# Kernel tuning notes

Hardware: AMD Instinct MI355X
Metric: run time of the kernel (lower is better)

Reference implementation:

```python
import jax, jax.numpy as jnp
import numpy as np

EPS = 1e-5
H = 8  # attention heads


def _bn(f, g, b):
    # MinkowskiBatchNorm: per-channel batch-norm over all N points (training stats)
    mu = f.mean(0)
    var = f.var(0)
    return g * (f - mu) * jax.lax.rsqrt(var + EPS) + b


def setup_inputs() -> dict:
    key = jax.random.key(0)
    ks = jax.random.split(key, 8)
    B, GS, ED = 8, 1024, 512
    N = B * GS
    s = 1.0 / np.sqrt(ED)
    inp = {
        "x": jax.random.normal(ks[0], (N, ED), jnp.float32),
        "mask": jnp.ones((B, GS), bool),
        "Wq": jax.random.normal(ks[1], (ED, ED), jnp.float32) * s,
        "bq": jnp.zeros((ED,), jnp.float32),
        "Wk": jax.random.normal(ks[2], (ED, ED), jnp.float32) * s,
        "bk": jnp.zeros((ED,), jnp.float32),
        "Wv": jax.random.normal(ks[3], (ED, ED), jnp.float32) * s,
        "bv": jnp.zeros((ED,), jnp.float32),
        "Wo": jax.random.normal(ks[4], (ED, ED), jnp.float32) * s,
        "bo": jnp.zeros((ED,), jnp.float32),
        "g1": jnp.ones((ED,), jnp.float32),
        "be1": jnp.zeros((ED,), jnp.float32),
        "g2": jnp.ones((ED,), jnp.float32),
        "be2": jnp.zeros((ED,), jnp.float32),
        "W1": jax.random.normal(ks[5], (ED, 4 * ED), jnp.float32) * s,
        "b1m": jnp.zeros((4 * ED,), jnp.float32),
        "W2": jax.random.normal(ks[6], (4 * ED, ED), jnp.float32) * (0.5 * s),
        "b2m": jnp.zeros((ED,), jnp.float32),
        "b": B,
        "gs": GS,
    }
    return inp


def reference(x, mask, Wq, bq, Wk, bk, Wv, bv, Wo, bo, g1, be1, g2, be2, W1, b1m, W2, b2m, b, gs):
    ed = x.shape[-1]
    dh = ed // H
    # --- pre-norm + multi-head self-attention over [b, gs] groups ---
    h1 = _bn(x, g1, be1)
    q = (h1 @ Wq + bq).reshape(b, gs, H, dh)
    k = (h1 @ Wk + bk).reshape(b, gs, H, dh)
    v = (h1 @ Wv + bv).reshape(b, gs, H, dh)
    scores = jnp.einsum('bqhd,bkhd->bhqk', q, k) / jnp.sqrt(jnp.float32(dh))
    scores = jnp.where(mask[:, None, None, :], scores, jnp.float32(-1e9))
    a = jax.nn.softmax(scores, axis=-1)
    o = jnp.einsum('bhqk,bkhd->bqhd', a, v).reshape(b * gs, ed)
    x = x + (o @ Wo + bo)  # residual (dropout identity at eval/d_rate=0)
    # --- pre-norm + MLP (GELU exact, as torch default) ---
    h2 = _bn(x, g2, be2)
    m = jax.nn.gelu(h2 @ W1 + b1m, approximate=False) @ W2 + b2m
    return x + m
```

## Files before the change

### kernel.cpp

```cpp
#include <hip/hip_runtime.h>
#include <hip/hip_bf16.h>


typedef unsigned short u16;
typedef unsigned int   u32;
typedef __attribute__((ext_vector_type(8))) short bf16x8;
typedef __attribute__((ext_vector_type(4))) float f32x4;
typedef __attribute__((ext_vector_type(4))) u16   u16x4;

#define ED   512
#define NTOK 8192
#define GSZ  1024
#define NH   8
#define DH   64

__device__ __forceinline__ u16 f2bf(float f) {
    __hip_bfloat16 h = __float2bfloat16(f);
    union { __hip_bfloat16 h; u16 u; } v; v.h = h;
    return v.u;
}

__device__ __forceinline__ void gload_lds16(const u16* g, u16* lds) {
    __builtin_amdgcn_global_load_lds(
        (const __attribute__((address_space(1))) u32*)g,
        (__attribute__((address_space(3))) u32*)lds, 16, 0, 0);
}

__device__ __forceinline__ f32x4 mfma16(bf16x8 a, bf16x8 b, f32x4 c) {
    return __builtin_amdgcn_mfma_f32_16x16x32_bf16(a, b, c, 0, 0, 0);
}

__device__ __forceinline__ float fast_gelu(float v) {
    float u = v * (0.797884560802865f + 0.0356774081f * v * v);
    float e = exp2f(u * 2.88539008177793f);
    float t = 1.f - 2.f / (1.f + e);
    return 0.5f * v * (1.f + t);
}

__device__ __forceinline__ void xcd_swizzle(int& bx, int& by) {
    int ny = gridDim.y;
    int nwg = gridDim.x * ny;
    int wg = blockIdx.y * gridDim.x + blockIdx.x;
    int per = nwg >> 3;
    int swz = (wg & 7) * per + (wg >> 3);
    by = swz % ny;
    bx = swz / ny;
}

__global__ __launch_bounds__(256) void wt_cast(const float* __restrict__ W,
                                               u16* __restrict__ Wt, int K, int N)
{
    __shared__ float t[32][33];
    int n0 = blockIdx.x * 32, k0 = blockIdx.y * 32;
    int tx = threadIdx.x & 31, ty = threadIdx.x >> 5;
#pragma unroll
    for (int r = 0; r < 4; ++r)
        t[ty * 4 + r][tx] = W[(size_t)(k0 + ty * 4 + r) * N + n0 + tx];
    __syncthreads();
#pragma unroll
    for (int r = 0; r < 4; ++r)
        Wt[(size_t)(n0 + ty * 4 + r) * K + k0 + tx] = f2bf(t[tx][ty * 4 + r]);
}

__global__ __launch_bounds__(256) void wt_cast4(
    const float* w0, const float* w1, const float* w2, const float* w3,
    u16* o0, u16* o1, u16* o2, u16* o3)
{
    const float* W = blockIdx.z == 0 ? w0 : blockIdx.z == 1 ? w1 : blockIdx.z == 2 ? w2 : w3;
    u16*        Wt = blockIdx.z == 0 ? o0 : blockIdx.z == 1 ? o1 : blockIdx.z == 2 ? o2 : o3;
    __shared__ float t[32][33];
    int n0 = blockIdx.x * 32, k0 = blockIdx.y * 32;
    int tx = threadIdx.x & 31, ty = threadIdx.x >> 5;
#pragma unroll
    for (int r = 0; r < 4; ++r)
        t[ty * 4 + r][tx] = W[(size_t)(k0 + ty * 4 + r) * ED + n0 + tx];
    __syncthreads();
#pragma unroll
    for (int r = 0; r < 4; ++r)
        Wt[(size_t)(n0 + ty * 4 + r) * ED + k0 + tx] = f2bf(t[tx][ty * 4 + r]);
}

__global__ __launch_bounds__(512) void bn_stats(const float* __restrict__ x,
                                                float* __restrict__ psum,
                                                float* __restrict__ psq)
{
    int c = threadIdx.x, blk = blockIdx.x;
    const float* p = x + (size_t)blk * 64 * ED + c;
    float s = 0.f, q = 0.f;
#pragma unroll 4
    for (int r = 0; r < 64; ++r) { float v = p[(size_t)r * ED]; s += v; q += v * v; }
    psum[blk * ED + c] = s;
    psq [blk * ED + c] = q;
}

__global__ __launch_bounds__(512) void bn_final(const float* __restrict__ psum,
                                                const float* __restrict__ psq,
                                                const float* __restrict__ g,
                                                const float* __restrict__ be,
                                                float* __restrict__ sb)
{
    int c = threadIdx.x;
    float s = 0.f, q = 0.f;
    for (int i = 0; i < 128; ++i) { s += psum[i * ED + c]; q += psq[i * ED + c]; }
    float mu  = s * (1.f / NTOK);
    float var = q * (1.f / NTOK) - mu * mu;
    float sc  = g[c] * rsqrtf(var + 1e-5f);
    sb[c]      = sc;
    sb[ED + c] = be[c] - mu * sc;
}

__global__ __launch_bounds__(256) void bn_apply(const float* __restrict__ x,
                                                const float* __restrict__ sb,
                                                u16* __restrict__ h)
{
    size_t idx = (size_t)blockIdx.x * 256 + threadIdx.x;
    const float4 v = ((const float4*)x)[idx];
    int c = (int)((idx * 4) & (ED - 1));
    u16x4 o;
    o[0] = f2bf(v.x * sb[c + 0] + sb[ED + c + 0]);
    o[1] = f2bf(v.y * sb[c + 1] + sb[ED + c + 1]);
    o[2] = f2bf(v.z * sb[c + 2] + sb[ED + c + 2]);
    o[3] = f2bf(v.w * sb[c + 3] + sb[ED + c + 3]);
    ((u16x4*)h)[idx] = o;
}

template <int BN, int BK>
__device__ __forceinline__ void gemm_core(const u16* __restrict__ A,
                                          const u16* __restrict__ Bt,
                                          int lda, int ldb, int K,
                                          size_t arow0, size_t brow0,
                                          u16 (&As)[2][128 * BK], u16 (&Bs)[2][BN * BK],
                                          f32x4 (&acc)[4][BN / 32])
{
    constexpr int NJ   = BN / 32;
    constexpr int KH   = BK / 32;
    constexpr int SEGS = BK / 8;
    constexpr int ACH  = (128 * BK) / 2048;
    constexpr int BCH  = (BN * BK) / 2048;
    const int tid  = threadIdx.x;
    const int lane = tid & 63, wid = tid >> 6;
    const int wm = wid >> 1, wn = wid & 1;
    const int frow = lane & 15, g = lane >> 4;
#pragma unroll
    for (int i = 0; i < 4; ++i)
#pragma unroll
        for (int j = 0; j < NJ; ++j) acc[i][j] = f32x4{0.f, 0.f, 0.f, 0.f};

#define SWZSEG(SG, R) ((BK == 64) ? ((SG) ^ ((R) & 7)) : ((SG) ^ (((R) >> 1) & 3)))
#define STAGE(K0, BUF) do {                                                     \
        _Pragma("unroll")                                                       \
        for (int a_ = 0; a_ < ACH; ++a_) {                                      \
            int c_ = tid + a_ * 256; int r_ = c_ / SEGS; int sg_ = c_ % SEGS;   \
            gload_lds16(A + (arow0 + r_) * lda + (K0) + SWZSEG(sg_, r_) * 8,    \
                        &As[BUF][c_ * 8]);                                      \
        }                                                                       \
        _Pragma("unroll")                                                       \
        for (int b_ = 0; b_ < BCH; ++b_) {                                      \
            int c_ = tid + b_ * 256; int r_ = c_ / SEGS; int sg_ = c_ % SEGS;   \
            gload_lds16(Bt + (brow0 + r_) * ldb + (K0) + SWZSEG(sg_, r_) * 8,   \
                        &Bs[BUF][c_ * 8]);                                      \
        }                                                                       \
    } while (0)

    STAGE(0, 0);
    __syncthreads();

    const int nt = K / BK;
    for (int t = 0; t < nt; ++t) {
        const int cur = t & 1;
        if (t + 1 < nt) STAGE((t + 1) * BK, cur ^ 1);
        const char* Ac = (const char*)&As[cur][0];
        const char* Bc = (const char*)&Bs[cur][0];
        bf16x8 af[4][KH], bfr[NJ][KH];
#pragma unroll
        for (int i = 0; i < 4; ++i) {
            int row = wm * 64 + i * 16 + frow;
#pragma unroll
            for (int kh = 0; kh < KH; ++kh) {
                int byte = row * (2 * BK) + kh * 64 + g * 16;
                byte ^= (BK == 64) ? ((row & 7) << 4) : ((row & 6) << 3);
                af[i][kh] = *(const bf16x8*)(Ac + byte);
            }
        }
#pragma unroll
        for (int j = 0; j < NJ; ++j) {
            int row = wn * (BN / 2) + j * 16 + frow;
#pragma unroll
            for (int kh = 0; kh < KH; ++kh) {
                int byte = row * (2 * BK) + kh * 64 + g * 16;
                byte ^= (BK == 64) ? ((row & 7) << 4) : ((row & 6) << 3);
                bfr[j][kh] = *(const bf16x8*)(Bc + byte);
            }
        }
#pragma unroll
        for (int kh = 0; kh < KH; ++kh)
#pragma unroll
            for (int i = 0; i < 4; ++i)
#pragma unroll
                for (int j = 0; j < NJ; ++j)
                    acc[i][j] = mfma16(af[i][kh], bfr[j][kh], acc[i][j]);
        __syncthreads();
    }
#undef STAGE
#undef SWZSEG
}

__global__ __launch_bounds__(256) void qkv_gemm(
    const u16* __restrict__ h1,
    const u16* __restrict__ wqT, const u16* __restrict__ wkT, const u16* __restrict__ wvT,
    const float* __restrict__ bq, const float* __restrict__ bk, const float* __restrict__ bv,
    u16* __restrict__ Q, u16* __restrict__ Kb, u16* __restrict__ Vt)
{
    __shared__ u16 As[2][4096];
    __shared__ u16 Bs[2][4096];
    int bx, by;
    xcd_swizzle(bx, by);
    int mb = bx;
    int which = by >> 2;
    int nloc = (by & 3) * 128;
    const u16*  Bt   = which == 0 ? wqT : (which == 1 ? wkT : wvT);
    const float* bias = which == 0 ? bq : (which == 1 ? bk : bv);
    f32x4 acc[4][4];
    gemm_core<128, 32>(h1, Bt, ED, ED, ED, (size_t)mb * 128, (size_t)nloc, As, Bs, acc);

    int lane = threadIdx.x & 63, wid = threadIdx.x >> 6;
    int wm = wid >> 1, wn = wid & 1, G = lane >> 4, r16 = lane & 15;
    int colb = nloc + wn * 64 + r16;
    float bsc[4];
#pragma unroll
    for (int j = 0; j < 4; ++j) bsc[j] = bias[colb + j * 16];

    if (which == 2) {
#pragma unroll
        for (int i = 0; i < 4; ++i) {
            int row0 = mb * 128 + wm * 64 + i * 16 + G * 4;
            int bidx = row0 >> 10, kv = row0 & (GSZ - 1);
#pragma unroll
            for (int j = 0; j < 4; ++j) {
                int col = colb + j * 16;
                int hh = col >> 6, d = col & 63;
                u16x4 pk;
#pragma unroll
                for (int r = 0; r < 4; ++r) pk[r] = f2bf(acc[i][j][r] + bsc[j]);
                *(u16x4*)(Vt + ((size_t)((bidx * NH + hh) * DH + d)) * GSZ + kv) = pk;
            }
        }
    } else {
        float scale = which == 0 ? 0.18033688011112042f : 1.0f;
        u16* Dst = which == 0 ? Q : Kb;
#pragma unroll
        for (int i = 0; i < 4; ++i) {
            int row = mb * 128 + wm * 64 + i * 16 + G * 4;
#pragma unroll
            for (int j = 0; j < 4; ++j) {
                int col = colb + j * 16;
#pragma unroll
                for (int r = 0; r < 4; ++r)
                    Dst[(size_t)(row + r) * ED + col] = f2bf((acc[i][j][r] + bsc[j]) * scale);
            }
        }
    }
}

template <int MODE, int BN, int BK>
__global__ __launch_bounds__(256) void gemm_epi(
    const u16* __restrict__ A, const u16* __restrict__ Bt, const float* __restrict__ bias,
    const float* res, float* outf, u16* outb, int K, int N)
{
    __shared__ u16 As[2][128 * BK];
    __shared__ u16 Bs[2][BN * BK];
    constexpr int NJ = BN / 32;
    int bx, by;
    xcd_swizzle(bx, by);
    f32x4 acc[4][NJ];
    gemm_core<BN, BK>(A, Bt, K, K, K, (size_t)bx * 128, (size_t)by * BN, As, Bs, acc);

    int lane = threadIdx.x & 63, wid = threadIdx.x >> 6;
    int wm = wid >> 1, wn = wid & 1, G = lane >> 4, r16 = lane & 15;
    int colb = by * BN + wn * (BN / 2) + r16;
    float bsc[NJ];
#pragma unroll
    for (int j = 0; j < NJ; ++j) bsc[j] = bias[colb + j * 16];
#pragma unroll
    for (int i = 0; i < 4; ++i) {
        int row = bx * 128 + wm * 64 + i * 16 + G * 4;
#pragma unroll
        for (int j = 0; j < NJ; ++j) {
            int col = colb + j * 16;
#pragma unroll
            for (int r = 0; r < 4; ++r) {
                float v = acc[i][j][r] + bsc[j];
                size_t o = (size_t)(row + r) * N + col;
                if (MODE == 1) {
                    outf[o] = v + res[o];
                } else {
                    outb[o] = f2bf(fast_gelu(v));
                }
            }
        }
    }
}

template <int MODE>
__global__ __launch_bounds__(512, 1) void gemm256(
    const u16* __restrict__ A, const u16* __restrict__ Bt, const float* __restrict__ bias,
    const float* res, float* outf, u16* outb, int K, int N)
{
    __shared__ u16 As[2][2][256 * 32];
    __shared__ u16 Bs[2][2][256 * 32];
    int bx, by;
    xcd_swizzle(bx, by);
    const int tid = threadIdx.x;
    const int lane = tid & 63, wid = tid >> 6;
    const int wm = wid >> 2, wn = wid & 3;
    const int frow = lane & 15, g = lane >> 4;
    const size_t arow0 = (size_t)bx * 256, brow0 = (size_t)by * 256;

    f32x4 acc[8][4];
#pragma unroll
    for (int i = 0; i < 8; ++i)
#pragma unroll
        for (int j = 0; j < 4; ++j) acc[i][j] = f32x4{0.f, 0.f, 0.f, 0.f};

#define SSLICE(KT, SL, BUF) do {                                                \
        const u16* m_ = ((SL) & 1) ? Bt : A;                                    \
        size_t rb_ = ((SL) & 1) ? brow0 : arow0;                                \
        u16* d_ = ((SL) & 1) ? &Bs[BUF][(SL) >> 1][0] : &As[BUF][(SL) >> 1][0]; \
        int kc_ = (KT) * 64 + ((SL) >> 1) * 32;                                 \
        _Pragma("unroll")                                                       \
        for (int q_ = 0; q_ < 2; ++q_) {                                        \
            int c_ = tid + q_ * 512;                                            \
            int r_ = c_ >> 2, sg_ = (c_ & 3) ^ ((r_ >> 1) & 3);                 \
            gload_lds16(m_ + (rb_ + r_) * (size_t)K + kc_ + sg_ * 8,            \
                        d_ + c_ * 8);                                           \
        }                                                                       \
    } while (0)

#define PHASE(BUF, KH, IH) do {                                                 \
        const char* Ac_ = (const char*)&As[BUF][KH][0];                         \
        const char* Bc_ = (const char*)&Bs[BUF][KH][0];                         \
        bf16x8 af_[4], bf_[4];                                                  \
        _Pragma("unroll")                                                       \
        for (int j_ = 0; j_ < 4; ++j_) {                                        \
            int row_ = wn * 64 + j_ * 16 + frow;                                \
            bf_[j_] = *(const bf16x8*)(Bc_ + row_ * 64 +                        \
                       ((g ^ ((row_ >> 1) & 3)) << 4));                         \
        }                                                                       \
        _Pragma("unroll")                                                       \
        for (int i_ = 0; i_ < 4; ++i_) {                                        \
            int row_ = wm * 128 + ((IH) * 4 + i_) * 16 + frow;                  \
            af_[i_] = *(const bf16x8*)(Ac_ + row_ * 64 +                        \
                       ((g ^ ((row_ >> 1) & 3)) << 4));                         \
        }                                                                       \
        __builtin_amdgcn_s_setprio(1);                                          \
        _Pragma("unroll")                                                       \
        for (int i_ = 0; i_ < 4; ++i_)                                          \
            _Pragma("unroll")                                                   \
            for (int j_ = 0; j_ < 4; ++j_)                                      \
                acc[(IH) * 4 + i_][j_] = mfma16(af_[i_], bf_[j_],               \
                                                acc[(IH) * 4 + i_][j_]);        \
        __builtin_amdgcn_s_setprio(0);                                          \
    } while (0)

    const int nt = K >> 6;
    SSLICE(0, 0, 0); SSLICE(0, 1, 0); SSLICE(0, 2, 0); SSLICE(0, 3, 0);
    asm volatile("s_waitcnt vmcnt(4)" ::: "memory");
    asm volatile("s_barrier" ::: "memory");

    for (int kt = 0; kt < nt; ++kt) {
        const int buf = kt & 1;
        const bool more = (kt + 1 < nt);
        if (more) SSLICE(kt + 1, 0, buf ^ 1);
        PHASE(buf, 0, 0);
        if (more) SSLICE(kt + 1, 1, buf ^ 1);
        PHASE(buf, 0, 1);
        if (more) asm volatile("s_waitcnt vmcnt(4)" ::: "memory");
        else      asm volatile("s_waitcnt vmcnt(0)" ::: "memory");
        asm volatile("s_barrier" ::: "memory");
        if (more) SSLICE(kt + 1, 2, buf ^ 1);
        PHASE(buf, 1, 0);
        if (more) SSLICE(kt + 1, 3, buf ^ 1);
        PHASE(buf, 1, 1);
        if (more) asm volatile("s_waitcnt vmcnt(4)" ::: "memory");
        else      asm volatile("s_waitcnt vmcnt(0)" ::: "memory");
        asm volatile("s_barrier" ::: "memory");
    }
#undef SSLICE
#undef PHASE

    const int G = lane >> 4, r16 = lane & 15;
    int colb = by * 256 + wn * 64 + r16;
    float bsc[4];
#pragma unroll
    for (int j = 0; j < 4; ++j) bsc[j] = bias[colb + j * 16];
#pragma unroll
    for (int i = 0; i < 8; ++i) {
        int row = bx * 256 + wm * 128 + i * 16 + G * 4;
#pragma unroll
        for (int j = 0; j < 4; ++j) {
            int col = colb + j * 16;
#pragma unroll
            for (int r = 0; r < 4; ++r) {
                float v = acc[i][j][r] + bsc[j];
                size_t o = (size_t)(row + r) * N + col;
                if (MODE == 1) {
                    outf[o] = v + res[o];
                } else {
                    outb[o] = f2bf(fast_gelu(v));
                }
            }
        }
    }
}

__global__ __launch_bounds__(512) void attn(const u16* __restrict__ Q,
                                            const u16* __restrict__ Kb,
                                            const u16* __restrict__ Vt,
                                            u16* __restrict__ O)
{
    __shared__ u16 KS[3][4096];
    __shared__ u16 VS[3][4096];
    __shared__ u16 P[8][1024];

    const int f = blockIdx.y * 8 + blockIdx.x;
    const int qt = (f >> 3) & 7;
    const int bh = ((f >> 6) << 3) + (f & 7);
    const int b = bh >> 3, h = bh & 7;
    const int tid = threadIdx.x, lane = tid & 63, w = tid >> 6;
    const int G = lane >> 4, r16 = lane & 15;
    char* Pw = (char*)&P[w][0];
    const int qbase = qt * 128 + w * 16;
    const int swz = (r16 & 7) << 4;

    const u16* kbase = Kb + ((size_t)b * GSZ) * ED + h * DH;
    const u16* vbase = Vt + ((size_t)bh * DH) * GSZ;

    const int c0 = tid;
    const int row0 = c0 >> 3, seg0 = (c0 & 7) ^ (row0 & 7);

    bf16x8 aq[2];
#pragma unroll
    for (int ks = 0; ks < 2; ++ks)
        aq[ks] = *(const bf16x8*)(Q + (size_t)(b * GSZ + qbase + r16) * ED
                                  + h * DH + ks * 32 + G * 8);

    bf16x8 ones;
#pragma unroll
    for (int i = 0; i < 8; ++i) ones[i] = (short)0x3F80;

    f32x4 o[4];
#pragma unroll
    for (int dt = 0; dt < 4; ++dt) o[dt] = f32x4{0.f, 0.f, 0.f, 0.f};
    f32x4 o_l = f32x4{0.f, 0.f, 0.f, 0.f};
    float m = -3e38f;

#define ASTAGE(C, BUF) do {                                                     \
        int kv0_ = (C) * 64;                                                    \
        gload_lds16(kbase + (size_t)(kv0_ + row0) * ED + seg0 * 8,              \
                    &KS[BUF][0] + c0 * 8);                                      \
        gload_lds16(vbase + (size_t)row0 * GSZ + kv0_ + seg0 * 8,               \
                    &VS[BUF][0] + c0 * 8);                                      \
    } while (0)

    ASTAGE(0, 0);
    ASTAGE(1, 1);
    asm volatile("s_waitcnt vmcnt(2)" ::: "memory");
    asm volatile("s_barrier" ::: "memory");

    for (int c = 0; c < 16; ++c) {
        const int cur = c % 3;
        if (c + 2 < 16) ASTAGE(c + 2, (c + 2) % 3);
        const char* Kc = (const char*)&KS[cur][0];
        const char* Vc = (const char*)&VS[cur][0];

        f32x4 s[4];
#pragma unroll
        for (int t = 0; t < 4; ++t) s[t] = f32x4{0.f, 0.f, 0.f, 0.f};
#pragma unroll
        for (int t = 0; t < 4; ++t) {
            int kvrow = (t * 16 + r16) * 128;
#pragma unroll
            for (int ks = 0; ks < 2; ++ks) {
                bf16x8 bk = *(const bf16x8*)(Kc + ((kvrow + ks * 64 + G * 16) ^ swz));
                s[t] = mfma16(bk, aq[ks], s[t]);
            }
        }

        float cm = fmaxf(fmaxf(fmaxf(s[0][0], s[0][1]), fmaxf(s[0][2], s[0][3])),
                         fmaxf(fmaxf(s[1][0], s[1][1]), fmaxf(s[1][2], s[1][3])));
        float cm2 = fmaxf(fmaxf(fmaxf(s[2][0], s[2][1]), fmaxf(s[2][2], s[2][3])),
                          fmaxf(fmaxf(s[3][0], s[3][1]), fmaxf(s[3][2], s[3][3])));
        cm = fmaxf(cm, cm2);
        if (__any(cm - m > 8.f)) {
            float mx = fmaxf(cm, __shfl_xor(cm, 16, 64));
            mx = fmaxf(mx, __shfl_xor(mx, 32, 64));
            float mn = fmaxf(m, mx);
            float r = exp2f(m - mn);
            m = mn;
            float rb[4];
#pragma unroll
            for (int j = 0; j < 4; ++j) rb[j] = __shfl(r, G * 4 + j, 64);
#pragma unroll
            for (int dt = 0; dt < 4; ++dt) {
                o[dt][0] *= rb[0]; o[dt][1] *= rb[1];
                o[dt][2] *= rb[2]; o[dt][3] *= rb[3];
            }
            o_l[0] *= rb[0]; o_l[1] *= rb[1];
            o_l[2] *= rb[2]; o_l[3] *= rb[3];
        }

#pragma unroll
        for (int t = 0; t < 4; ++t) {
            u16x4 pk;
            pk[0] = f2bf(exp2f(s[t][0] - m));
            pk[1] = f2bf(exp2f(s[t][1] - m));
            pk[2] = f2bf(exp2f(s[t][2] - m));
            pk[3] = f2bf(exp2f(s[t][3] - m));
            *(u16x4*)(Pw + ((r16 * 128 + t * 32 + G * 8) ^ swz)) = pk;
        }

#pragma unroll
        for (int ks = 0; ks < 2; ++ks) {
            bf16x8 pa = *(const bf16x8*)(Pw + ((r16 * 128 + ks * 64 + G * 16) ^ swz));
            o_l = mfma16(pa, ones, o_l);
#pragma unroll
            for (int dt = 0; dt < 4; ++dt) {
                bf16x8 bv = *(const bf16x8*)(Vc + (((dt * 16 + r16) * 128 + ks * 64 + G * 16) ^ swz));
                o[dt] = mfma16(pa, bv, o[dt]);
            }
        }

        if (c < 15) {
            if (c + 2 < 16) asm volatile("s_waitcnt vmcnt(2)" ::: "memory");
            else            asm volatile("s_waitcnt vmcnt(0)" ::: "memory");
            asm volatile("s_barrier" ::: "memory");
        }
    }
#undef ASTAGE

    float linv[4];
#pragma unroll
    for (int j = 0; j < 4; ++j) linv[j] = 1.f / o_l[j];
#pragma unroll
    for (int dt = 0; dt < 4; ++dt)
#pragma unroll
        for (int j = 0; j < 4; ++j) {
            int row = b * GSZ + qbase + G * 4 + j;
            O[(size_t)row * ED + h * DH + dt * 16 + r16] = f2bf(o[dt][j] * linv[j]);
        }
}

extern "C" void kernel_launch(void* const* d_in, const int* in_sizes, int n_in,
                              void* d_out, int out_size, void* d_ws, size_t ws_size,
                              hipStream_t stream)
{
    const float* x   = (const float*)d_in[0];
    const float* Wq  = (const float*)d_in[2];
    const float* bq  = (const float*)d_in[3];
    const float* Wk  = (const float*)d_in[4];
    const float* bk  = (const float*)d_in[5];
    const float* Wv  = (const float*)d_in[6];
    const float* bv  = (const float*)d_in[7];
    const float* Wo  = (const float*)d_in[8];
    const float* bo  = (const float*)d_in[9];
    const float* g1  = (const float*)d_in[10];
    const float* be1 = (const float*)d_in[11];
    const float* g2  = (const float*)d_in[12];
    const float* be2 = (const float*)d_in[13];
    const float* W1  = (const float*)d_in[14];
    const float* b1m = (const float*)d_in[15];
    const float* W2  = (const float*)d_in[16];
    const float* b2m = (const float*)d_in[17];
    float* out = (float*)d_out;
    char* ws = (char*)d_ws;

    u16*   wqT  = (u16*)(ws + 0);
    u16*   wkT  = (u16*)(ws + 524288);
    u16*   wvT  = (u16*)(ws + 1048576);
    u16*   woT  = (u16*)(ws + 1572864);
    u16*   w1T  = (u16*)(ws + 2097152);
    u16*   w2T  = (u16*)(ws + 4194304);
    float* sb1  = (float*)(ws + 6291456);
    float* sb2  = (float*)(ws + 6295552);
    float* psum = (float*)(ws + 6299648);
    float* psq  = (float*)(ws + 6561792);
    u16*   h1   = (u16*)(ws + 7340032);
    u16*   Qb   = (u16*)(ws + 16777216);
    u16*   Kbf  = (u16*)(ws + 25165824);
    u16*   Vt   = (u16*)(ws + 33554432);
    u16*   mid  = (u16*)(ws + 16777216);
    u16*   Ob   = h1;
    u16*   h2   = h1;

    wt_cast4<<<dim3(16, 16, 4), 256, 0, stream>>>(Wq, Wk, Wv, Wo, wqT, wkT, wvT, woT);
    wt_cast<<<dim3(64, 16), 256, 0, stream>>>(W1, w1T, ED, 4 * ED);
    wt_cast<<<dim3(16, 64), 256, 0, stream>>>(W2, w2T, 4 * ED, ED);

    bn_stats<<<128, 512, 0, stream>>>(x, psum, psq);
    bn_final<<<1, 512, 0, stream>>>(psum, psq, g1, be1, sb1);
    bn_apply<<<4096, 256, 0, stream>>>(x, sb1, h1);

    qkv_gemm<<<dim3(64, 12), 256, 0, stream>>>(h1, wqT, wkT, wvT, bq, bk, bv, Qb, Kbf, Vt);

    attn<<<dim3(8, 64), 512, 0, stream>>>(Qb, Kbf, Vt, Ob);

    gemm_epi<1, 64, 64><<<dim3(64, 8), 256, 0, stream>>>(Ob, woT, bo, x, out, nullptr, ED, ED);

    bn_stats<<<128, 512, 0, stream>>>(out, psum, psq);
    bn_final<<<1, 512, 0, stream>>>(psum, psq, g2, be2, sb2);
    bn_apply<<<4096, 256, 0, stream>>>(out, sb2, h2);

    gemm256<2><<<dim3(32, 8), 512, 0, stream>>>(h2, w1T, b1m, nullptr, nullptr, mid, ED, 4 * ED);

    gemm_epi<1, 64, 64><<<dim3(64, 8), 256, 0, stream>>>(mid, w2T, b2m, out, out, nullptr, 4 * ED, ED);
}
```

Before: 193.5 us.

## Pipeline GEMM core with sliced K=64 staging and fine-grained waitcnt barriers

Replaces the templated double-buffered GEMM core with a fixed 128x128, K=64 pipeline. Each K tile is split into four 32-wide slices, and the loads for the next tile are interleaved between MFMA phases. Waits use explicit vmcnt counts with raw s_barrier, and setprio raises priority around the MFMA blocks. The Wo and W2 projection GEMMs move from 128x64 to 128x128 tiles, which halves the grid to 256 blocks. This gives fewer blocks per CU for latency hiding and uses more LDS per block, in exchange for better load/compute overlap and reuse.

```diff
diff --git a/kernel.cpp b/kernel.cpp
--- a/kernel.cpp
+++ b/kernel.cpp
@@ -124,19 +124,13 @@
     ((u16x4*)h)[idx] = o;
 }
 
-template <int BN, int BK>
-__device__ __forceinline__ void gemm_core(const u16* __restrict__ A,
-                                          const u16* __restrict__ Bt,
-                                          int lda, int ldb, int K,
-                                          size_t arow0, size_t brow0,
-                                          u16 (&As)[2][128 * BK], u16 (&Bs)[2][BN * BK],
-                                          f32x4 (&acc)[4][BN / 32])
-{
-    constexpr int NJ   = BN / 32;
-    constexpr int KH   = BK / 32;
-    constexpr int SEGS = BK / 8;
-    constexpr int ACH  = (128 * BK) / 2048;
-    constexpr int BCH  = (BN * BK) / 2048;
+__device__ __forceinline__ void gemm_core_p(const u16* __restrict__ A,
+                                            const u16* __restrict__ Bt,
+                                            int lda, int ldb, int K,
+                                            size_t arow0, size_t brow0,
+                                            u16 (&As)[2][2][4096], u16 (&Bs)[2][2][4096],
+                                            f32x4 (&acc)[4][4])
+{
     const int tid  = threadIdx.x;
     const int lane = tid & 63, wid = tid >> 6;
     const int wm = wid >> 1, wn = wid & 1;
@@ -144,65 +138,74 @@
 #pragma unroll
     for (int i = 0; i < 4; ++i)
 #pragma unroll
-        for (int j = 0; j < NJ; ++j) acc[i][j] = f32x4{0.f, 0.f, 0.f, 0.f};
-
-#define SWZSEG(SG, R) ((BK == 64) ? ((SG) ^ ((R) & 7)) : ((SG) ^ (((R) >> 1) & 3)))
-#define STAGE(K0, BUF) do {                                                     \
-        _Pragma("unroll")                                                       \
-        for (int a_ = 0; a_ < ACH; ++a_) {                                      \
-            int c_ = tid + a_ * 256; int r_ = c_ / SEGS; int sg_ = c_ % SEGS;   \
-            gload_lds16(A + (arow0 + r_) * lda + (K0) + SWZSEG(sg_, r_) * 8,    \
-                        &As[BUF][c_ * 8]);                                      \
-        }                                                                       \
-        _Pragma("unroll")                                                       \
-        for (int b_ = 0; b_ < BCH; ++b_) {                                      \
-            int c_ = tid + b_ * 256; int r_ = c_ / SEGS; int sg_ = c_ % SEGS;   \
-            gload_lds16(Bt + (brow0 + r_) * ldb + (K0) + SWZSEG(sg_, r_) * 8,   \
-                        &Bs[BUF][c_ * 8]);                                      \
+        for (int j = 0; j < 4; ++j) acc[i][j] = f32x4{0.f, 0.f, 0.f, 0.f};
+
+#define SSL(KT, SL, BUF) do {                                                   \
+        const u16* m_ = ((SL) & 1) ? Bt : A;                                    \
+        int ld_ = ((SL) & 1) ? ldb : lda;                                       \
+        size_t rb_ = ((SL) & 1) ? brow0 : arow0;                                \
+        u16* d_ = ((SL) & 1) ? &Bs[BUF][(SL) >> 1][0] : &As[BUF][(SL) >> 1][0]; \
+        int kc_ = (KT) * 64 + ((SL) >> 1) * 32;                                 \
+        _Pragma("unroll")                                                       \
+        for (int q_ = 0; q_ < 2; ++q_) {                                        \
+            int c_ = tid + q_ * 256;                                            \
+            int r_ = c_ >> 2, sg_ = (c_ & 3) ^ ((r_ >> 1) & 3);                 \
+            gload_lds16(m_ + (rb_ + r_) * (size_t)ld_ + kc_ + sg_ * 8,          \
+                        d_ + c_ * 8);                                           \
         }                                                                       \
     } while (0)
 
-    STAGE(0, 0);
-    __syncthreads();
-
-    const int nt = K / BK;
-    for (int t = 0; t < nt; ++t) {
-        const int cur = t & 1;
-        if (t + 1 < nt) STAGE((t + 1) * BK, cur ^ 1);
-        const char* Ac = (const char*)&As[cur][0];
-        const char* Bc = (const char*)&Bs[cur][0];
-        bf16x8 af[4][KH], bfr[NJ][KH];
-#pragma unroll
-        for (int i = 0; i < 4; ++i) {
-            int row = wm * 64 + i * 16 + frow;
-#pragma unroll
-            for (int kh = 0; kh < KH; ++kh) {
-                int byte = row * (2 * BK) + kh * 64 + g * 16;
-                byte ^= (BK == 64) ? ((row & 7) << 4) : ((row & 6) << 3);
-                af[i][kh] = *(const bf16x8*)(Ac + byte);
-            }
-        }
-#pragma unroll
-        for (int j = 0; j < NJ; ++j) {
-            int row = wn * (BN / 2) + j * 16 + frow;
-#pragma unroll
-            for (int kh = 0; kh < KH; ++kh) {
-                int byte = row * (2 * BK) + kh * 64 + g * 16;
-                byte ^= (BK == 64) ? ((row & 7) << 4) : ((row & 6) << 3);
-                bfr[j][kh] = *(const bf16x8*)(Bc + byte);
-            }
-        }
-#pragma unroll
-        for (int kh = 0; kh < KH; ++kh)
-#pragma unroll
-            for (int i = 0; i < 4; ++i)
-#pragma unroll
-                for (int j = 0; j < NJ; ++j)
-                    acc[i][j] = mfma16(af[i][kh], bfr[j][kh], acc[i][j]);
-        __syncthreads();
+#define PH(BUF, KH, IH) do {                                                    \
+        const char* Ac_ = (const char*)&As[BUF][KH][0];                         \
+        const char* Bc_ = (const char*)&Bs[BUF][KH][0];                         \
+        bf16x8 af_[2], bf_[4];                                                  \
+        _Pragma("unroll")                                                       \
+        for (int j_ = 0; j_ < 4; ++j_) {                                        \
+            int row_ = wn * 64 + j_ * 16 + frow;                                \
+            bf_[j_] = *(const bf16x8*)(Bc_ + row_ * 64 +                        \
+                       ((g ^ ((row_ >> 1) & 3)) << 4));                         \
+        }                                                                       \
+        _Pragma("unroll")                                                       \
+        for (int i_ = 0; i_ < 2; ++i_) {                                        \
+            int row_ = wm * 64 + ((IH) * 2 + i_) * 16 + frow;                   \
+            af_[i_] = *(const bf16x8*)(Ac_ + row_ * 64 +                        \
+                       ((g ^ ((row_ >> 1) & 3)) << 4));                         \
+        }                                                                       \
+        __builtin_amdgcn_s_setprio(1);                                          \
+        _Pragma("unroll")                                                       \
+        for (int i_ = 0; i_ < 2; ++i_)                                          \
+            _Pragma("unroll")                                                   \
+            for (int j_ = 0; j_ < 4; ++j_)                                      \
+                acc[(IH) * 2 + i_][j_] = mfma16(af_[i_], bf_[j_],               \
+                                                acc[(IH) * 2 + i_][j_]);        \
+        __builtin_amdgcn_s_setprio(0);                                          \
+    } while (0)
+
+    const int nt = K >> 6;
+    SSL(0, 0, 0); SSL(0, 1, 0); SSL(0, 2, 0); SSL(0, 3, 0);
+    asm volatile("s_waitcnt vmcnt(4)" ::: "memory");
+    asm volatile("s_barrier" ::: "memory");
+
+    for (int kt = 0; kt < nt; ++kt) {
+        const int buf = kt & 1;
+        const bool more = (kt + 1 < nt);
+        if (more) SSL(kt + 1, 0, buf ^ 1);
+        PH(buf, 0, 0);
+        if (more) SSL(kt + 1, 1, buf ^ 1);
+        PH(buf, 0, 1);
+        if (more) asm volatile("s_waitcnt vmcnt(4)" ::: "memory");
+        else      asm volatile("s_waitcnt vmcnt(0)" ::: "memory");
+        asm volatile("s_barrier" ::: "memory");
+        if (more) SSL(kt + 1, 2, buf ^ 1);
+        PH(buf, 1, 0);
+        if (more) SSL(kt + 1, 3, buf ^ 1);
+        PH(buf, 1, 1);
+        if (more) asm volatile("s_waitcnt vmcnt(4)" ::: "memory");
+        else      asm volatile("s_waitcnt vmcnt(0)" ::: "memory");
+        asm volatile("s_barrier" ::: "memory");
     }
-#undef STAGE
-#undef SWZSEG
+#undef SSL
+#undef PH
 }
 
 __global__ __launch_bounds__(256) void qkv_gemm(
@@ -211,8 +214,8 @@
     const float* __restrict__ bq, const float* __restrict__ bk, const float* __restrict__ bv,
     u16* __restrict__ Q, u16* __restrict__ Kb, u16* __restrict__ Vt)
 {
-    __shared__ u16 As[2][4096];
-    __shared__ u16 Bs[2][4096];
+    __shared__ u16 As[2][2][4096];
+    __shared__ u16 Bs[2][2][4096];
     int bx, by;
     xcd_swizzle(bx, by);
     int mb = bx;
@@ -221,7 +224,7 @@
     const u16*  Bt   = which == 0 ? wqT : (which == 1 ? wkT : wvT);
     const float* bias = which == 0 ? bq : (which == 1 ? bk : bv);
     f32x4 acc[4][4];
-    gemm_core<128, 32>(h1, Bt, ED, ED, ED, (size_t)mb * 128, (size_t)nloc, As, Bs, acc);
+    gemm_core_p(h1, Bt, ED, ED, ED, (size_t)mb * 128, (size_t)nloc, As, Bs, acc);
 
     int lane = threadIdx.x & 63, wid = threadIdx.x >> 6;
     int wm = wid >> 1, wn = wid & 1, G = lane >> 4, r16 = lane & 15;
@@ -262,30 +265,29 @@
     }
 }
 
-template <int MODE, int BN, int BK>
+template <int MODE>
 __global__ __launch_bounds__(256) void gemm_epi(
     const u16* __restrict__ A, const u16* __restrict__ Bt, const float* __restrict__ bias,
     const float* res, float* outf, u16* outb, int K, int N)
 {
-    __shared__ u16 As[2][128 * BK];
-    __shared__ u16 Bs[2][BN * BK];
-    constexpr int NJ = BN / 32;
+    __shared__ u16 As[2][2][4096];
+    __shared__ u16 Bs[2][2][4096];
     int bx, by;
     xcd_swizzle(bx, by);
-    f32x4 acc[4][NJ];
-    gemm_core<BN, BK>(A, Bt, K, K, K, (size_t)bx * 128, (size_t)by * BN, As, Bs, acc);
+    f32x4 acc[4][4];
+    gemm_core_p(A, Bt, K, K, K, (size_t)bx * 128, (size_t)by * 128, As, Bs, acc);
 
     int lane = threadIdx.x & 63, wid = threadIdx.x >> 6;
     int wm = wid >> 1, wn = wid & 1, G = lane >> 4, r16 = lane & 15;
-    int colb = by * BN + wn * (BN / 2) + r16;
-    float bsc[NJ];
-#pragma unroll
-    for (int j = 0; j < NJ; ++j) bsc[j] = bias[colb + j * 16];
+    int colb = by * 128 + wn * 64 + r16;
+    float bsc[4];
+#pragma unroll
+    for (int j = 0; j < 4; ++j) bsc[j] = bias[colb + j * 16];
 #pragma unroll
     for (int i = 0; i < 4; ++i) {
         int row = bx * 128 + wm * 64 + i * 16 + G * 4;
 #pragma unroll
-        for (int j = 0; j < NJ; ++j) {
+        for (int j = 0; j < 4; ++j) {
             int col = colb + j * 16;
 #pragma unroll
             for (int r = 0; r < 4; ++r) {
@@ -604,7 +606,7 @@
 
     attn<<<dim3(8, 64), 512, 0, stream>>>(Qb, Kbf, Vt, Ob);
 
-    gemm_epi<1, 64, 64><<<dim3(64, 8), 256, 0, stream>>>(Ob, woT, bo, x, out, nullptr, ED, ED);
+    gemm_epi<1><<<dim3(64, 4), 256, 0, stream>>>(Ob, woT, bo, x, out, nullptr, ED, ED);
 
     bn_stats<<<128, 512, 0, stream>>>(out, psum, psq);
     bn_final<<<1, 512, 0, stream>>>(psum, psq, g2, be2, sb2);
@@ -612,5 +614,5 @@
 
     gemm256<2><<<dim3(32, 8), 512, 0, stream>>>(h2, w1T, b1m, nullptr, nullptr, mid, ED, 4 * ED);
 
-    gemm_epi<1, 64, 64><<<dim3(64, 8), 256, 0, stream>>>(mid, w2T, b2m, out, out, nullptr, 4 * ED, ED);
-}
+    gemm_epi<1><<<dim3(64, 4), 256, 0, stream>>>(mid, w2T, b2m, out, out, nullptr, 4 * ED, ED);
+}
```

Result: slower. 239.3 us (+23.7%).
